# Kernel tuning notes

Measured on AMD Instinct MI355X. Metric: run time of the kernel, lower is better.

Reference implementation:

```python
import jax, jax.numpy as jnp
import numpy as np

B, T, C = 4, 4096, 1024
DEGREE, EXPAND = 2, 2
H = EXPAND * C  # selector / inner dim = 2048


def setup_inputs() -> dict:
    key = jax.random.key(0)
    ks = jax.random.split(key, 4)
    sc = lambda d: 1.0 / np.sqrt(d)
    return {
        "x": jax.random.normal(ks[0], (B, T, C), jnp.float32),
        "W_sel": jax.random.normal(ks[1], (C, H), jnp.float32) * sc(C),
        "W_agg": jax.random.normal(ks[2], (C, DEGREE * H), jnp.float32) * sc(C),
        "W_out": jax.random.normal(ks[3], (H, C), jnp.float32) * sc(H),
        "sqk_q": jnp.ones((H,), jnp.float32),
        "sqk_k": jnp.ones((DEGREE * H,), jnp.float32),
    }


def reference(x, W_sel, W_agg, W_out, sqk_q, sqk_k):
    # Selector branch on queries (gated): B,T,H
    s = jax.nn.silu(jnp.einsum('btc,ch->bth', x, W_sel) * sqk_q)
    # Aggregator branch on context: B,T,DEGREE*H
    h = jnp.einsum('btc,cd->btd', x, W_agg) * sqk_k
    chunks = jnp.split(h, DEGREE, axis=-1)
    # Polynomial expansion: sum_{d=1..DEGREE} prod_{k<=d} chunk_k  -> B,T,H
    p = chunks[0]
    poly = p
    for c in chunks[1:]:
        p = p * c
        poly = poly + p
    # Causal masked mean: tril(ones(T,T)) @ poly / row-count == cumsum / arange.
    # Honors the causal structure without materializing the T x T mask.
    denom = jnp.arange(1, T + 1, dtype=poly.dtype)[None, :, None]
    agg = jnp.cumsum(poly, axis=1) / denom  # B,T,H causal running mean
    # Mix selected queries with aggregated polynomial state, project out.
    return jnp.einsum('bth,hc->btc', s * agg, W_out)
```

## Files before the change

kernel.cpp:

```cpp
#include <hip/hip_runtime.h>
#include <hip/hip_bf16.h>
#include <stdint.h>

#define BB 4
#define TT 4096
#define CC 1024
#define HH 2048
#define MM (BB*TT)
#define NCK 32
#define CKS 128

using short8 = __attribute__((ext_vector_type(8))) short;
using f32x4  = __attribute__((ext_vector_type(4))) float;

__device__ __forceinline__ unsigned short f2bf(float f) {
    union { float f; uint32_t u; } v; v.f = f;
    uint32_t r = v.u + 0x7fffu + ((v.u >> 16) & 1u);
    return (unsigned short)(r >> 16);
}
__device__ __forceinline__ float bf_lo(uint32_t u) {
    union { uint32_t u; float f; } v; v.u = u << 16; return v.f;
}
__device__ __forceinline__ float bf_hi(uint32_t u) {
    union { uint32_t u; float f; } v; v.u = u & 0xFFFF0000u; return v.f;
}
__device__ __forceinline__ uint32_t pack2bf(float lo, float hi) {
    return ((uint32_t)f2bf(lo)) | (((uint32_t)f2bf(hi)) << 16);
}

__global__ void conv_x_kernel(const float* __restrict__ x, unsigned short* __restrict__ xb, int n4) {
    int i = blockIdx.x * blockDim.x + threadIdx.x;
    if (i >= n4) return;
    float4 v = ((const float4*)x)[i];
    ushort4 o;
    o.x = f2bf(v.x); o.y = f2bf(v.y); o.z = f2bf(v.z); o.w = f2bf(v.w);
    ((ushort4*)xb)[i] = o;
}

__global__ void trans_direct_kernel(const float* __restrict__ in, unsigned short* __restrict__ out,
                                    const float* __restrict__ scale, int R, int Cin) {
    __shared__ float tile[32][33];
    int c0 = blockIdx.x * 32, k0 = blockIdx.y * 32;
    int tx = threadIdx.x;
    for (int i = threadIdx.y; i < 32; i += 8) {
        float s = scale ? scale[c0 + tx] : 1.f;
        tile[i][tx] = in[(size_t)(k0 + i) * Cin + c0 + tx] * s;
    }
    __syncthreads();
    for (int i = threadIdx.y; i < 32; i += 8)
        out[(size_t)(c0 + i) * R + k0 + tx] = f2bf(tile[tx][i]);
}

__global__ void trans_pair_kernel(const float* __restrict__ in, unsigned short* __restrict__ out,
                                  const float* __restrict__ scale) {
    __shared__ float tile[32][33];
    int q0 = blockIdx.x * 32, k0 = blockIdx.y * 32;
    int g = q0 >> 5;
    int tx = threadIdx.x;
    int c = (tx < 16) ? (g * 16 + tx) : (2048 + g * 16 + tx - 16);
    float s = scale[c];
    for (int i = threadIdx.y; i < 32; i += 8)
        tile[i][tx] = in[(size_t)(k0 + i) * 4096 + c] * s;
    __syncthreads();
    for (int i = threadIdx.y; i < 32; i += 8)
        out[(size_t)(q0 + i) * 1024 + k0 + tx] = f2bf(tile[tx][i]);
}

__global__ __launch_bounds__(256) void gemm_fused_kernel(
    const unsigned short* __restrict__ A,
    const unsigned short* __restrict__ Bt,
    unsigned short* __restrict__ Sout,
    unsigned short* __restrict__ Pout,
    float* __restrict__ part)
{
    __shared__ __align__(16) unsigned short As[128 * 64];
    __shared__ __align__(16) unsigned short Bs[128 * 64];
    __shared__ float psum[64];

    const int mt = blockIdx.x / 48;
    const int nt = blockIdx.x % 48;
    const int m0 = mt << 7, n0 = nt << 7;

    const int tid  = threadIdx.x;
    const int lane = tid & 63;
    const int wave = tid >> 6;
    const int l15  = lane & 15;
    const int quad = lane >> 4;
    const int wm = (wave >> 1) * 64;
    const int wn = (wave & 1) * 64;

    f32x4 acc[4][4];
#pragma unroll
    for (int i = 0; i < 4; i++)
#pragma unroll
        for (int j = 0; j < 4; j++) acc[i][j] = {0.f, 0.f, 0.f, 0.f};

    for (int k0 = 0; k0 < 1024; k0 += 64) {
#pragma unroll
        for (int it = 0; it < 4; it++) {
            int c  = it * 256 + tid;
            int r  = c >> 3;
            int sl = (c & 7) ^ (r & 7);
            const unsigned short* ga = A  + (size_t)(m0 + r) * 1024 + k0 + sl * 8;
            const unsigned short* gb = Bt + (size_t)(n0 + r) * 1024 + k0 + sl * 8;
            __builtin_amdgcn_global_load_lds(
                (const __attribute__((address_space(1))) void*)ga,
                (__attribute__((address_space(3))) void*)&As[c * 8], 16, 0, 0);
            __builtin_amdgcn_global_load_lds(
                (const __attribute__((address_space(1))) void*)gb,
                (__attribute__((address_space(3))) void*)&Bs[c * 8], 16, 0, 0);
        }
        __syncthreads();

#pragma unroll
        for (int ks = 0; ks < 2; ks++) {
            short8 af[4], bf[4];
#pragma unroll
            for (int i = 0; i < 4; i++) {
                int row = wm + i * 16 + l15;
                int ph = (quad + ks * 4) ^ (row & 7);
                af[i] = *(const short8*)&As[row * 64 + ph * 8];
            }
#pragma unroll
            for (int j = 0; j < 4; j++) {
                int row = wn + j * 16 + l15;
                int ph = (quad + ks * 4) ^ (row & 7);
                bf[j] = *(const short8*)&Bs[row * 64 + ph * 8];
            }
#pragma unroll
            for (int i = 0; i < 4; i++)
#pragma unroll
                for (int j = 0; j < 4; j++)
                    acc[i][j] = __builtin_amdgcn_mfma_f32_16x16x32_bf16(af[i], bf[j], acc[i][j], 0, 0, 0);
        }
        __syncthreads();
    }

    if (nt < 16) {
#pragma unroll
        for (int i = 0; i < 4; i++)
#pragma unroll
            for (int j = 0; j < 4; j++) {
                int col = n0 + wn + j * 16 + l15;
#pragma unroll
                for (int r = 0; r < 4; r++) {
                    int row = m0 + wm + i * 16 + quad * 4 + r;
                    float v = acc[i][j][r];
                    v = v / (1.f + __expf(-v));
                    Sout[(size_t)row * 2048 + col] = f2bf(v);
                }
            }
    } else {
        if (tid < 64) psum[tid] = 0.f;
        __syncthreads();
        int pbase = ((n0 - 2048 + wn) >> 1);
        float lsum0 = 0.f, lsum1 = 0.f;
#pragma unroll
        for (int i = 0; i < 4; i++) {
#pragma unroll
            for (int j = 0; j < 4; j += 2) {
                int pcol = pbase + (j >> 1) * 16 + l15;
#pragma unroll
                for (int r = 0; r < 4; r++) {
                    int row = m0 + wm + i * 16 + quad * 4 + r;
                    float pv = acc[i][j][r] * (1.f + acc[i][j + 1][r]);
                    Pout[(size_t)row * 2048 + pcol] = f2bf(pv);
                    if (j == 0) lsum0 += pv; else lsum1 += pv;
                }
            }
        }
        int pcl = (wn >> 1) + l15;
        atomicAdd(&psum[pcl], lsum0);
        atomicAdd(&psum[pcl + 16], lsum1);
        __syncthreads();
        if (tid < 64) {
            int b = m0 >> 12, ck = (m0 & 4095) >> 7;
            part[((size_t)b * NCK + ck) * 2048 + ((n0 - 2048) >> 1) + tid] = psum[tid];
        }
    }
}

__global__ __launch_bounds__(256) void gemm_out_kernel(
    const unsigned short* __restrict__ A,
    const unsigned short* __restrict__ Bt,
    float* __restrict__ Cout)
{
    __shared__ __align__(16) unsigned short As[128 * 64];
    __shared__ __align__(16) unsigned short Bs[128 * 64];

    const int mt = blockIdx.x >> 3;
    const int nt = blockIdx.x & 7;
    const int m0 = mt << 7, n0 = nt << 7;

    const int tid  = threadIdx.x;
    const int lane = tid & 63;
    const int wave = tid >> 6;
    const int l15  = lane & 15;
    const int quad = lane >> 4;
    const int wm = (wave >> 1) * 64;
    const int wn = (wave & 1) * 64;

    f32x4 acc[4][4];
#pragma unroll
    for (int i = 0; i < 4; i++)
#pragma unroll
        for (int j = 0; j < 4; j++) acc[i][j] = {0.f, 0.f, 0.f, 0.f};

    for (int k0 = 0; k0 < 2048; k0 += 64) {
#pragma unroll
        for (int it = 0; it < 4; it++) {
            int c  = it * 256 + tid;
            int r  = c >> 3;
            int sl = (c & 7) ^ (r & 7);
            const unsigned short* ga = A  + (size_t)(m0 + r) * 2048 + k0 + sl * 8;
            const unsigned short* gb = Bt + (size_t)(n0 + r) * 2048 + k0 + sl * 8;
            __builtin_amdgcn_global_load_lds(
                (const __attribute__((address_space(1))) void*)ga,
                (__attribute__((address_space(3))) void*)&As[c * 8], 16, 0, 0);
            __builtin_amdgcn_global_load_lds(
                (const __attribute__((address_space(1))) void*)gb,
                (__attribute__((address_space(3))) void*)&Bs[c * 8], 16, 0, 0);
        }
        __syncthreads();

#pragma unroll
        for (int ks = 0; ks < 2; ks++) {
            short8 af[4], bf[4];
#pragma unroll
            for (int i = 0; i < 4; i++) {
                int row = wm + i * 16 + l15;
                int ph = (quad + ks * 4) ^ (row & 7);
                af[i] = *(const short8*)&As[row * 64 + ph * 8];
            }
#pragma unroll
            for (int j = 0; j < 4; j++) {
                int row = wn + j * 16 + l15;
                int ph = (quad + ks * 4) ^ (row & 7);
                bf[j] = *(const short8*)&Bs[row * 64 + ph * 8];
            }
#pragma unroll
            for (int i = 0; i < 4; i++)
#pragma unroll
                for (int j = 0; j < 4; j++)
                    acc[i][j] = __builtin_amdgcn_mfma_f32_16x16x32_bf16(af[i], bf[j], acc[i][j], 0, 0, 0);
        }
        __syncthreads();
    }

#pragma unroll
    for (int i = 0; i < 4; i++)
#pragma unroll
        for (int j = 0; j < 4; j++) {
            int col = n0 + wn + j * 16 + l15;
#pragma unroll
            for (int r = 0; r < 4; r++) {
                int row = m0 + wm + i * 16 + quad * 4 + r;
                Cout[(size_t)row * 1024 + col] = acc[i][j][r];
            }
        }
}

__global__ void chunk_scan_kernel(float* __restrict__ part) {
    int idx = blockIdx.x * blockDim.x + threadIdx.x;
    int b = idx >> 11, col = idx & 2047;
    float run = 0.f;
    for (int ck = 0; ck < NCK; ck++) {
        size_t off = ((size_t)b * NCK + ck) * 2048 + col;
        float v = part[off];
        part[off] = run;
        run += v;
    }
}

__global__ void finalize_kernel(unsigned short* __restrict__ poly, const unsigned short* __restrict__ s,
                                const float* __restrict__ part) {
    int seg = blockIdx.x & 3;
    int ck  = (blockIdx.x >> 2) & (NCK - 1);
    int b   = blockIdx.x >> 7;
    int cp  = seg * 256 + threadIdx.x;
    size_t po = ((size_t)b * NCK + ck) * 2048 + cp * 2;
    float run0 = part[po], run1 = part[po + 1];
    size_t base = ((size_t)b * TT + (size_t)ck * CKS) * 2048 + cp * 2;
    for (int t = 0; t < CKS; t++) {
        int tg = ck * CKS + t;
        size_t off = base + (size_t)t * 2048;
        uint32_t pv = *(const uint32_t*)&poly[off];
        run0 += bf_lo(pv);
        run1 += bf_hi(pv);
        float inv = 1.f / (float)(tg + 1);
        uint32_t sv = *(const uint32_t*)&s[off];
        float m0 = bf_lo(sv) * run0 * inv;
        float m1 = bf_hi(sv) * run1 * inv;
        *(uint32_t*)&poly[off] = pack2bf(m0, m1);
    }
}

extern "C" void kernel_launch(void* const* d_in, const int* in_sizes, int n_in,
                              void* d_out, int out_size, void* d_ws, size_t ws_size,
                              hipStream_t stream) {
    const float* x     = (const float*)d_in[0];
    const float* W_sel = (const float*)d_in[1];
    const float* W_agg = (const float*)d_in[2];
    const float* W_out = (const float*)d_in[3];
    const float* sqk_q = (const float*)d_in[4];
    const float* sqk_k = (const float*)d_in[5];
    float* out = (float*)d_out;

    char* ws = (char*)d_ws;
    unsigned short* xb    = (unsigned short*)(ws);
    unsigned short* wallT = (unsigned short*)(ws + 33554432ull);
    unsigned short* woutT = (unsigned short*)(ws + 46137344ull);
    unsigned short* s_b   = (unsigned short*)(ws + 50331648ull);
    unsigned short* poly  = (unsigned short*)(ws + 117440512ull);
    float*          part  = (float*)(ws + 184549376ull);

    dim3 tb(32, 8);
    conv_x_kernel<<<(MM * CC / 4 + 255) / 256, 256, 0, stream>>>(x, xb, MM * CC / 4);
    trans_direct_kernel<<<dim3(HH / 32, CC / 32), tb, 0, stream>>>(W_sel, wallT, sqk_q, CC, HH);
    trans_pair_kernel<<<dim3(4096 / 32, CC / 32), tb, 0, stream>>>(W_agg, wallT + 2048ull * 1024, sqk_k);
    trans_direct_kernel<<<dim3(CC / 32, HH / 32), tb, 0, stream>>>(W_out, woutT, nullptr, HH, CC);

    gemm_fused_kernel<<<(MM / 128) * 48, 256, 0, stream>>>(xb, wallT, s_b, poly, part);

    chunk_scan_kernel<<<(BB * HH) / 256, 256, 0, stream>>>(part);
    finalize_kernel<<<BB * NCK * 4, 256, 0, stream>>>(poly, s_b, part);

    gemm_out_kernel<<<(MM / 128) * (CC / 128), 256, 0, stream>>>(poly, woutT, out);
}
```

Before: 549.6 us.

## Use 256x256 tiles with 4-stage LDS prefetch pipeline in both GEMMs

Both GEMMs now share one core that uses 256x256 block tiles with 512 threads (8 waves, each computing a 128x64 sub-tile). K-slices of 32 are staged into a 4-deep LDS ring buffer, with global_load_lds issued two tiles ahead and interleaved with MFMA phases via explicit barriers, waitcnt and setprio. The intent is to hide global-load latency and raise arithmetic intensity per LDS byte. In exchange it uses more LDS and registers per block, and there are fewer blocks to fill the CUs. The fused-epilogue partial sums are adapted to write two 128-row chunks per block.

```diff
diff --git a/kernel.cpp b/kernel.cpp
--- a/kernel.cpp
+++ b/kernel.cpp
@@ -66,79 +66,137 @@
         out[(size_t)(q0 + i) * 1024 + k0 + tx] = f2bf(tile[tx][i]);
 }
 
-__global__ __launch_bounds__(256) void gemm_fused_kernel(
+template<int LDK, int NT>
+__device__ __forceinline__ void gemm_core(
+    const unsigned short* __restrict__ A,
+    const unsigned short* __restrict__ Bt,
+    int m0, int n0, int tid,
+    f32x4 (&acc)[8][4])
+{
+    __shared__ __align__(16) unsigned short As[4 * 8192];
+    __shared__ __align__(16) unsigned short Bs[4 * 8192];
+
+    const int lane = tid & 63;
+    const int wave = tid >> 6;
+    const int l15  = lane & 15;
+    const int quad = lane >> 4;
+    const int wm = (wave >> 2) << 7;
+    const int wn = (wave & 3) << 6;
+
+#pragma unroll
+    for (int i = 0; i < 8; i++)
+#pragma unroll
+        for (int j = 0; j < 4; j++) acc[i][j] = {0.f, 0.f, 0.f, 0.f};
+
+    const int rl  = tid >> 2;
+    const int kc8 = ((tid & 3) ^ ((tid >> 3) & 3)) << 3;
+    const unsigned short* gA = A  + (size_t)(m0 + rl) * LDK + kc8;
+    const unsigned short* gB = Bt + (size_t)(n0 + rl) * LDK + kc8;
+
+#define STAGE(G, L) __builtin_amdgcn_global_load_lds( \
+        (const __attribute__((address_space(1))) void*)(G), \
+        (__attribute__((address_space(3))) void*)(L), 16, 0, 0)
+
+#pragma unroll
+    for (int t = 0; t < 2; t++) {
+        STAGE(gA + t * 32,             &As[t * 8192 + tid * 8]);
+        STAGE(gA + 128 * LDK + t * 32, &As[t * 8192 + 4096 + tid * 8]);
+        STAGE(gB + t * 32,             &Bs[t * 8192 + tid * 8]);
+        STAGE(gB + 128 * LDK + t * 32, &Bs[t * 8192 + 4096 + tid * 8]);
+    }
+    asm volatile("s_waitcnt vmcnt(4)" ::: "memory");
+    __builtin_amdgcn_s_barrier();
+
+    for (int t = 0; t < NT; ++t) {
+        const unsigned short* as = &As[(t & 3) * 8192];
+        const unsigned short* bs = &Bs[(t & 3) * 8192];
+        unsigned short* asd = &As[((t + 2) & 3) * 8192];
+        unsigned short* bsd = &Bs[((t + 2) & 3) * 8192];
+        const bool pf = (t + 2) < NT;
+
+        short8 af[4], bf[4];
+#pragma unroll
+        for (int i = 0; i < 4; i++) {
+            int row = wm + i * 16 + l15;
+            af[i] = *(const short8*)(as + row * 32 + ((quad ^ ((row >> 1) & 3)) << 3));
+        }
+#pragma unroll
+        for (int j = 0; j < 4; j++) {
+            int row = wn + j * 16 + l15;
+            bf[j] = *(const short8*)(bs + row * 32 + ((quad ^ ((row >> 1) & 3)) << 3));
+        }
+        if (pf) {
+            STAGE(gA + (t + 2) * 32,             asd + tid * 8);
+            STAGE(gA + 128 * LDK + (t + 2) * 32, asd + 4096 + tid * 8);
+        }
+        __builtin_amdgcn_s_barrier();
+        asm volatile("s_waitcnt lgkmcnt(0)" ::: "memory");
+        __builtin_amdgcn_sched_barrier(0);
+        __builtin_amdgcn_s_setprio(1);
+#pragma unroll
+        for (int i = 0; i < 4; i++)
+#pragma unroll
+            for (int j = 0; j < 4; j++)
+                acc[i][j] = __builtin_amdgcn_mfma_f32_16x16x32_bf16(af[i], bf[j], acc[i][j], 0, 0, 0);
+        __builtin_amdgcn_s_setprio(0);
+        __builtin_amdgcn_sched_barrier(0);
+        __builtin_amdgcn_s_barrier();
+
+        short8 ag[4];
+#pragma unroll
+        for (int i = 0; i < 4; i++) {
+            int row = wm + 64 + i * 16 + l15;
+            ag[i] = *(const short8*)(as + row * 32 + ((quad ^ ((row >> 1) & 3)) << 3));
+        }
+        if (pf) {
+            STAGE(gB + (t + 2) * 32,             bsd + tid * 8);
+            STAGE(gB + 128 * LDK + (t + 2) * 32, bsd + 4096 + tid * 8);
+        }
+        __builtin_amdgcn_s_barrier();
+        asm volatile("s_waitcnt lgkmcnt(0)" ::: "memory");
+        __builtin_amdgcn_sched_barrier(0);
+        __builtin_amdgcn_s_setprio(1);
+#pragma unroll
+        for (int i = 0; i < 4; i++)
+#pragma unroll
+            for (int j = 0; j < 4; j++)
+                acc[4 + i][j] = __builtin_amdgcn_mfma_f32_16x16x32_bf16(ag[i], bf[j], acc[4 + i][j], 0, 0, 0);
+        __builtin_amdgcn_s_setprio(0);
+        __builtin_amdgcn_sched_barrier(0);
+        if (t < NT - 2) { asm volatile("s_waitcnt vmcnt(4)" ::: "memory"); }
+        else            { asm volatile("s_waitcnt vmcnt(0)" ::: "memory"); }
+        __builtin_amdgcn_s_barrier();
+    }
+#undef STAGE
+}
+
+__global__ __launch_bounds__(512, 2) void gemm_fused_kernel(
     const unsigned short* __restrict__ A,
     const unsigned short* __restrict__ Bt,
     unsigned short* __restrict__ Sout,
     unsigned short* __restrict__ Pout,
     float* __restrict__ part)
 {
-    __shared__ __align__(16) unsigned short As[128 * 64];
-    __shared__ __align__(16) unsigned short Bs[128 * 64];
-    __shared__ float psum[64];
-
-    const int mt = blockIdx.x / 48;
-    const int nt = blockIdx.x % 48;
-    const int m0 = mt << 7, n0 = nt << 7;
-
-    const int tid  = threadIdx.x;
+    __shared__ float psum[256];
+    const int tid = threadIdx.x;
+    const int mt = blockIdx.x / 24;
+    const int nt = blockIdx.x % 24;
+    const int m0 = mt << 8, n0 = nt << 8;
+    if (tid < 256) psum[tid] = 0.f;
+
+    f32x4 acc[8][4];
+    gemm_core<1024, 32>(A, Bt, m0, n0, tid, acc);
+
     const int lane = tid & 63;
     const int wave = tid >> 6;
     const int l15  = lane & 15;
     const int quad = lane >> 4;
-    const int wm = (wave >> 1) * 64;
-    const int wn = (wave & 1) * 64;
-
-    f32x4 acc[4][4];
-#pragma unroll
-    for (int i = 0; i < 4; i++)
-#pragma unroll
-        for (int j = 0; j < 4; j++) acc[i][j] = {0.f, 0.f, 0.f, 0.f};
-
-    for (int k0 = 0; k0 < 1024; k0 += 64) {
-#pragma unroll
-        for (int it = 0; it < 4; it++) {
-            int c  = it * 256 + tid;
-            int r  = c >> 3;
-            int sl = (c & 7) ^ (r & 7);
-            const unsigned short* ga = A  + (size_t)(m0 + r) * 1024 + k0 + sl * 8;
-            const unsigned short* gb = Bt + (size_t)(n0 + r) * 1024 + k0 + sl * 8;
-            __builtin_amdgcn_global_load_lds(
-                (const __attribute__((address_space(1))) void*)ga,
-                (__attribute__((address_space(3))) void*)&As[c * 8], 16, 0, 0);
-            __builtin_amdgcn_global_load_lds(
-                (const __attribute__((address_space(1))) void*)gb,
-                (__attribute__((address_space(3))) void*)&Bs[c * 8], 16, 0, 0);
-        }
-        __syncthreads();
-
-#pragma unroll
-        for (int ks = 0; ks < 2; ks++) {
-            short8 af[4], bf[4];
-#pragma unroll
-            for (int i = 0; i < 4; i++) {
-                int row = wm + i * 16 + l15;
-                int ph = (quad + ks * 4) ^ (row & 7);
-                af[i] = *(const short8*)&As[row * 64 + ph * 8];
-            }
-#pragma unroll
-            for (int j = 0; j < 4; j++) {
-                int row = wn + j * 16 + l15;
-                int ph = (quad + ks * 4) ^ (row & 7);
-                bf[j] = *(const short8*)&Bs[row * 64 + ph * 8];
-            }
-#pragma unroll
-            for (int i = 0; i < 4; i++)
-#pragma unroll
-                for (int j = 0; j < 4; j++)
-                    acc[i][j] = __builtin_amdgcn_mfma_f32_16x16x32_bf16(af[i], bf[j], acc[i][j], 0, 0, 0);
-        }
-        __syncthreads();
-    }
-
-    if (nt < 16) {
-#pragma unroll
-        for (int i = 0; i < 4; i++)
+    const int wm = (wave >> 2) << 7;
+    const int wn = (wave & 3) << 6;
+
+    if (nt < 8) {
+#pragma unroll
+        for (int i = 0; i < 8; i++)
 #pragma unroll
             for (int j = 0; j < 4; j++) {
                 int col = n0 + wn + j * 16 + l15;
@@ -151,104 +209,55 @@
                 }
             }
     } else {
-        if (tid < 64) psum[tid] = 0.f;
-        __syncthreads();
-        int pbase = ((n0 - 2048 + wn) >> 1);
+        const int pbase = ((n0 - 2048 + wn) >> 1);
         float lsum0 = 0.f, lsum1 = 0.f;
 #pragma unroll
-        for (int i = 0; i < 4; i++) {
-#pragma unroll
-            for (int j = 0; j < 4; j += 2) {
-                int pcol = pbase + (j >> 1) * 16 + l15;
+        for (int i = 0; i < 8; i++) {
+#pragma unroll
+            for (int jp = 0; jp < 2; jp++) {
+                int pcol = pbase + jp * 16 + l15;
 #pragma unroll
                 for (int r = 0; r < 4; r++) {
                     int row = m0 + wm + i * 16 + quad * 4 + r;
-                    float pv = acc[i][j][r] * (1.f + acc[i][j + 1][r]);
+                    float pv = acc[i][2 * jp][r] * (1.f + acc[i][2 * jp + 1][r]);
                     Pout[(size_t)row * 2048 + pcol] = f2bf(pv);
-                    if (j == 0) lsum0 += pv; else lsum1 += pv;
+                    if (jp == 0) lsum0 += pv; else lsum1 += pv;
                 }
             }
         }
-        int pcl = (wn >> 1) + l15;
-        atomicAdd(&psum[pcl], lsum0);
-        atomicAdd(&psum[pcl + 16], lsum1);
+        int base = (wm >> 7) * 128 + (wn >> 1) + l15;
+        atomicAdd(&psum[base], lsum0);
+        atomicAdd(&psum[base + 16], lsum1);
         __syncthreads();
-        if (tid < 64) {
-            int b = m0 >> 12, ck = (m0 & 4095) >> 7;
-            part[((size_t)b * NCK + ck) * 2048 + ((n0 - 2048) >> 1) + tid] = psum[tid];
-        }
-    }
-}
-
-__global__ __launch_bounds__(256) void gemm_out_kernel(
+        if (tid < 256) {
+            int b  = m0 >> 12;
+            int ck = ((m0 & 4095) >> 7) + (tid >> 7);
+            part[((size_t)b * NCK + ck) * 2048 + ((n0 - 2048) >> 1) + (tid & 127)] = psum[tid];
+        }
+    }
+}
+
+__global__ __launch_bounds__(512, 2) void gemm_out_kernel(
     const unsigned short* __restrict__ A,
     const unsigned short* __restrict__ Bt,
     float* __restrict__ Cout)
 {
-    __shared__ __align__(16) unsigned short As[128 * 64];
-    __shared__ __align__(16) unsigned short Bs[128 * 64];
-
-    const int mt = blockIdx.x >> 3;
-    const int nt = blockIdx.x & 7;
-    const int m0 = mt << 7, n0 = nt << 7;
-
-    const int tid  = threadIdx.x;
+    const int tid = threadIdx.x;
+    const int mt = blockIdx.x >> 2;
+    const int nt = blockIdx.x & 3;
+    const int m0 = mt << 8, n0 = nt << 8;
+
+    f32x4 acc[8][4];
+    gemm_core<2048, 64>(A, Bt, m0, n0, tid, acc);
+
     const int lane = tid & 63;
     const int wave = tid >> 6;
     const int l15  = lane & 15;
     const int quad = lane >> 4;
-    const int wm = (wave >> 1) * 64;
-    const int wn = (wave & 1) * 64;
-
-    f32x4 acc[4][4];
-#pragma unroll
-    for (int i = 0; i < 4; i++)
-#pragma unroll
-        for (int j = 0; j < 4; j++) acc[i][j] = {0.f, 0.f, 0.f, 0.f};
-
-    for (int k0 = 0; k0 < 2048; k0 += 64) {
-#pragma unroll
-        for (int it = 0; it < 4; it++) {
-            int c  = it * 256 + tid;
-            int r  = c >> 3;
-            int sl = (c & 7) ^ (r & 7);
-            const unsigned short* ga = A  + (size_t)(m0 + r) * 2048 + k0 + sl * 8;
-            const unsigned short* gb = Bt + (size_t)(n0 + r) * 2048 + k0 + sl * 8;
-            __builtin_amdgcn_global_load_lds(
-                (const __attribute__((address_space(1))) void*)ga,
-                (__attribute__((address_space(3))) void*)&As[c * 8], 16, 0, 0);
-            __builtin_amdgcn_global_load_lds(
-                (const __attribute__((address_space(1))) void*)gb,
-                (__attribute__((address_space(3))) void*)&Bs[c * 8], 16, 0, 0);
-        }
-        __syncthreads();
-
-#pragma unroll
-        for (int ks = 0; ks < 2; ks++) {
-            short8 af[4], bf[4];
-#pragma unroll
-            for (int i = 0; i < 4; i++) {
-                int row = wm + i * 16 + l15;
-                int ph = (quad + ks * 4) ^ (row & 7);
-                af[i] = *(const short8*)&As[row * 64 + ph * 8];
-            }
-#pragma unroll
-            for (int j = 0; j < 4; j++) {
-                int row = wn + j * 16 + l15;
-                int ph = (quad + ks * 4) ^ (row & 7);
-                bf[j] = *(const short8*)&Bs[row * 64 + ph * 8];
-            }
-#pragma unroll
-            for (int i = 0; i < 4; i++)
-#pragma unroll
-                for (int j = 0; j < 4; j++)
-                    acc[i][j] = __builtin_amdgcn_mfma_f32_16x16x32_bf16(af[i], bf[j], acc[i][j], 0, 0, 0);
-        }
-        __syncthreads();
-    }
-
-#pragma unroll
-    for (int i = 0; i < 4; i++)
+    const int wm = (wave >> 2) << 7;
+    const int wn = (wave & 3) << 6;
+#pragma unroll
+    for (int i = 0; i < 8; i++)
 #pragma unroll
         for (int j = 0; j < 4; j++) {
             int col = n0 + wn + j * 16 + l15;
@@ -320,10 +329,10 @@
     trans_pair_kernel<<<dim3(4096 / 32, CC / 32), tb, 0, stream>>>(W_agg, wallT + 2048ull * 1024, sqk_k);
     trans_direct_kernel<<<dim3(CC / 32, HH / 32), tb, 0, stream>>>(W_out, woutT, nullptr, HH, CC);
 
-    gemm_fused_kernel<<<(MM / 128) * 48, 256, 0, stream>>>(xb, wallT, s_b, poly, part);
+    gemm_fused_kernel<<<(MM / 256) * 24, 512, 0, stream>>>(xb, wallT, s_b, poly, part);
 
     chunk_scan_kernel<<<(BB * HH) / 256, 256, 0, stream>>>(part);
     finalize_kernel<<<BB * NCK * 4, 256, 0, stream>>>(poly, s_b, part);
 
-    gemm_out_kernel<<<(MM / 128) * (CC / 128), 256, 0, stream>>>(poly, woutT, out);
-}
+    gemm_out_kernel<<<(MM / 256) * (CC / 256), 512, 0, stream>>>(poly, woutT, out);
+}
```

Result: faster. 473.0 us (-13.9%).
